# Optimization experiments

Hardware: AMD Instinct MI355X
Metric: run time of the kernel (lower is better)

Reference implementation:

```python
import jax, jax.numpy as jnp
import numpy as np

H = 512   # hidden_size
E = 256   # embedding_size
V = 32000 # vocab_size
L = 1024  # max_length (encoder seq len)
B = 64    # batch


def setup_inputs() -> dict:
    key = jax.random.key(0)
    ks = jax.random.split(key, 18)
    n = lambda i, shape, s=0.05: (jax.random.normal(ks[i], shape, dtype=jnp.float32) * s)
    return {
        "input": jax.random.randint(ks[0], (B, 1), 0, V),
        "last_output_context": n(1, (1, B, H), 1.0),
        "last_hidden": n(2, (1, B, H), 1.0),
        "last_cell_state": n(3, (1, B, H), 1.0),
        "encoder_outputs": n(4, (L, B, H), 1.0),
        "emb": n(5, (V, E)),
        "W_ih": n(6, (4 * H, E + H)),
        "W_hh": n(7, (4 * H, H)),
        "b_ih": n(8, (4 * H,)),
        "b_hh": n(9, (4 * H,)),
        "W_attn": n(10, (H, 2 * H)),
        "b_attn": n(11, (H,)),
        "beta": n(12, (H, 1), 1.0),
        "W_oc": n(13, (H, 2 * H)),
        "b_oc": n(14, (H,)),
        "W_out": n(15, (V, H)),
        "b_out": n(16, (V,)),
    }


def reference(input, last_output_context, last_hidden, last_cell_state,
              encoder_outputs, emb, W_ih, W_hh, b_ih, b_hh,
              W_attn, b_attn, beta, W_oc, b_oc, W_out, b_out):
    # embedding lookup: (B,1) -> (B,E)  (permute(1,0,2) then squeeze step dim)
    tok = emb[input[:, 0]]                                   # (B, E)
    x = jnp.concatenate([tok, last_output_context[0]], axis=1)  # (B, E+H)
    # single-step LSTM (PyTorch gate order i, f, g, o)
    gates = x @ W_ih.T + last_hidden[0] @ W_hh.T + b_ih + b_hh  # (B, 4H)
    i_g, f_g, g_g, o_g = jnp.split(gates, 4, axis=1)
    i_g = jax.nn.sigmoid(i_g)
    f_g = jax.nn.sigmoid(f_g)
    g_g = jnp.tanh(g_g)
    o_g = jax.nn.sigmoid(o_g)
    c = f_g * last_cell_state[0] + i_g * g_g                  # (B, H)
    h = o_g * jnp.tanh(c)                                     # (B, H) == rnn_output
    # additive attention, vectorized over the seq_len loop
    h_tiled = jnp.broadcast_to(h[None], (L, B, H))
    cat = jnp.concatenate([h_tiled, encoder_outputs], axis=-1)  # (L, B, 2H)
    energy = jnp.tanh(cat @ W_attn.T + b_attn) @ beta           # (L, B, 1)
    attn_w = jax.nn.softmax(energy[..., 0], axis=0)             # (L, B) softmax over seq
    # context = bmm(attn_weights, encoder_outputs)
    context = jnp.einsum('lb,lbh->bh', attn_w, encoder_outputs)  # (B, H)
    co = jnp.tanh(jnp.concatenate([h, context], axis=1) @ W_oc.T + b_oc)  # (B, H)
    output = jax.nn.log_softmax(co @ W_out.T + b_out, axis=1)    # (B, V)
    return output, co[None], h[None], c[None]
```

## Files before the change

### kernel.cpp

```cpp
#include <hip/hip_runtime.h>
#include <hip/hip_bf16.h>
#include <cstddef>

#define H   512
#define E   256
#define V   32000
#define L   1024
#define B   64
#define KX  768
#define M_TOT 65536

typedef __attribute__((ext_vector_type(8))) _Float16 half8v;
typedef __attribute__((ext_vector_type(4))) float f32x4;

__device__ __forceinline__ half8v cvt8(float4 x0, float4 x1) {
    union { half8v v; _Float16 u[8]; } hv;
    hv.u[0] = (_Float16)x0.x; hv.u[1] = (_Float16)x0.y;
    hv.u[2] = (_Float16)x0.z; hv.u[3] = (_Float16)x0.w;
    hv.u[4] = (_Float16)x1.x; hv.u[5] = (_Float16)x1.y;
    hv.u[6] = (_Float16)x1.z; hv.u[7] = (_Float16)x1.w;
    return hv.v;
}

__global__ __launch_bounds__(256) void k_conv_w(const float* __restrict__ W_attn,
                                                unsigned short* __restrict__ Wf) {
    int e0 = blockIdx.x * 2048 + threadIdx.x * 8;
    int j = e0 >> 9, k = e0 & 511;
    const float* src = &W_attn[(size_t)j * (2 * H) + H + k];
    float4 x0 = *reinterpret_cast<const float4*>(src);
    float4 x1 = *reinterpret_cast<const float4*>(src + 4);
    half8v hv = cvt8(x0, x1);
    *reinterpret_cast<half8v*>(&Wf[e0]) = hv;
}

__global__ __launch_bounds__(256) void k_build(const int* __restrict__ inp,
                                               const float* __restrict__ loc,
                                               const float* __restrict__ hprev,
                                               const float* __restrict__ emb,
                                               float* __restrict__ xprevT) {
    int gid = blockIdx.x * 256 + threadIdx.x;
    int k = gid >> 6, b = gid & 63;
    float v;
    if (k < 256)      v = emb[(size_t)inp[b] * E + k];
    else if (k < 768) v = loc[b * H + (k - 256)];
    else              v = hprev[b * H + (k - 768)];
    xprevT[gid] = v;
}

__global__ __launch_bounds__(256) void k_lstm(const float* __restrict__ W_ih,
                                              const float* __restrict__ W_hh,
                                              const float* __restrict__ b_ih,
                                              const float* __restrict__ b_hh,
                                              const float* __restrict__ xprevT,
                                              const float* __restrict__ cprev,
                                              float* __restrict__ h_out,
                                              float* __restrict__ c_out,
                                              float* __restrict__ hnewT) {
    int u = blockIdx.x;
    int w = threadIdx.x >> 6;
    int b = threadIdx.x & 63;
    int j = w * 512 + u;
    float a0 = 0.f, a1 = 0.f, a2 = 0.f, a3 = 0.f;
    const float* Wr = &W_ih[(size_t)j * KX];
    for (int k = 0; k < KX; k += 4) {
        float4 wv = *reinterpret_cast<const float4*>(&Wr[k]);
        a0 += wv.x * xprevT[(k + 0) * 64 + b];
        a1 += wv.y * xprevT[(k + 1) * 64 + b];
        a2 += wv.z * xprevT[(k + 2) * 64 + b];
        a3 += wv.w * xprevT[(k + 3) * 64 + b];
    }
    const float* Wr2 = &W_hh[(size_t)j * H];
    const float* hT = &xprevT[KX * 64];
    for (int k = 0; k < H; k += 4) {
        float4 wv = *reinterpret_cast<const float4*>(&Wr2[k]);
        a0 += wv.x * hT[(k + 0) * 64 + b];
        a1 += wv.y * hT[(k + 1) * 64 + b];
        a2 += wv.z * hT[(k + 2) * 64 + b];
        a3 += wv.w * hT[(k + 3) * 64 + b];
    }
    float acc = b_ih[j] + b_hh[j] + ((a0 + a1) + (a2 + a3));
    __shared__ float gs[4][64];
    gs[w][b] = acc;
    __syncthreads();
    if (threadIdx.x < 64) {
        float ig = 1.f / (1.f + __expf(-gs[0][b]));
        float fg = 1.f / (1.f + __expf(-gs[1][b]));
        float gg = tanhf(gs[2][b]);
        float og = 1.f / (1.f + __expf(-gs[3][b]));
        float c = fg * cprev[b * H + u] + ig * gg;
        float h = og * tanhf(c);
        c_out[b * H + u] = c;
        h_out[b * H + u] = h;
        hnewT[u * 64 + b] = h;
    }
}

__global__ __launch_bounds__(256) void k_hw(const float* __restrict__ W_attn,
                                            const float* __restrict__ b_attn,
                                            const float* __restrict__ hT,
                                            float* __restrict__ hW_jb) {
    int j = blockIdx.x * 4 + (threadIdx.x >> 6);
    int b = threadIdx.x & 63;
    float a0 = 0.f, a1 = 0.f, a2 = 0.f, a3 = 0.f;
    const float* Wr = &W_attn[(size_t)j * (2 * H)];
    for (int k = 0; k < H; k += 4) {
        float4 wv = *reinterpret_cast<const float4*>(&Wr[k]);
        a0 += wv.x * hT[(k + 0) * 64 + b];
        a1 += wv.y * hT[(k + 1) * 64 + b];
        a2 += wv.z * hT[(k + 2) * 64 + b];
        a3 += wv.w * hT[(k + 3) * 64 + b];
    }
    hW_jb[j * 64 + b] = b_attn[j] + ((a0 + a1) + (a2 + a3));
}

#define BKE 32
#define PITCH 40

__global__ __launch_bounds__(256, 4) void k_energy_v7(
        const float* __restrict__ enc,
        const unsigned short* __restrict__ Wf,
        const float* __restrict__ hW,
        const float* __restrict__ beta,
        float* __restrict__ partial_e) {
    __shared__ unsigned short Ah[128 * PITCH];
    __shared__ unsigned short Bh[128 * PITCH];
    __shared__ float red[2][128];

    const int tid  = threadIdx.x;
    const int lane = tid & 63;
    const int wave = tid >> 6;
    const int wm = wave >> 1;
    const int wn = wave & 1;
    const int bid = blockIdx.x;
    const int xcd = bid & 7;
    const int loc = bid >> 3;
    const int mt  = xcd * 64 + (loc >> 2);
    const int jt  = loc & 3;
    const int m0 = mt * 128;
    const int j0 = jt * 128;

    const int srow = tid >> 2;
    const int skc  = tid & 3;

    float4 ra0[2], ra1[2];
    half8v rb[2];
    #pragma unroll
    for (int p = 0; p < 2; ++p) {
        int row = p * 64 + srow;
        const float* asrc = &enc[(size_t)(m0 + row) * H + skc * 8];
        ra0[p] = *reinterpret_cast<const float4*>(asrc);
        ra1[p] = *reinterpret_cast<const float4*>(asrc + 4);
        rb[p] = *reinterpret_cast<const half8v*>(&Wf[(size_t)(j0 + row) * H + skc * 8]);
    }

    f32x4 acc[4][4];
    #pragma unroll
    for (int i = 0; i < 4; ++i)
        #pragma unroll
        for (int j = 0; j < 4; ++j) acc[i][j] = (f32x4){0.f, 0.f, 0.f, 0.f};

    for (int k0 = 0; k0 < H; k0 += BKE) {
        __syncthreads();
        #pragma unroll
        for (int p = 0; p < 2; ++p) {
            half8v hv = cvt8(ra0[p], ra1[p]);
            int off = (p * 64 + srow) * PITCH + skc * 8;
            *reinterpret_cast<half8v*>(&Ah[off]) = hv;
            *reinterpret_cast<half8v*>(&Bh[off]) = rb[p];
        }
        __syncthreads();
        if (k0 + BKE < H) {
            int kn = k0 + BKE;
            #pragma unroll
            for (int p = 0; p < 2; ++p) {
                int row = p * 64 + srow;
                const float* asrc = &enc[(size_t)(m0 + row) * H + kn + skc * 8];
                ra0[p] = *reinterpret_cast<const float4*>(asrc);
                ra1[p] = *reinterpret_cast<const float4*>(asrc + 4);
                rb[p] = *reinterpret_cast<const half8v*>(&Wf[(size_t)(j0 + row) * H + kn + skc * 8]);
            }
        }
        const int fr = lane & 15;
        const int kb = (lane >> 4) * 8;
        half8v a_h[4], b_h[4];
        #pragma unroll
        for (int mf = 0; mf < 4; ++mf) {
            int off = (wm * 64 + mf * 16 + fr) * PITCH + kb;
            a_h[mf] = *reinterpret_cast<const half8v*>(&Ah[off]);
        }
        #pragma unroll
        for (int nf = 0; nf < 4; ++nf) {
            int off = (wn * 64 + nf * 16 + fr) * PITCH + kb;
            b_h[nf] = *reinterpret_cast<const half8v*>(&Bh[off]);
        }
        #pragma unroll
        for (int mf = 0; mf < 4; ++mf)
            #pragma unroll
            for (int nf = 0; nf < 4; ++nf)
                acc[mf][nf] = __builtin_amdgcn_mfma_f32_16x16x32_f16(
                    a_h[mf], b_h[nf], acc[mf][nf], 0, 0, 0);
    }
    float psum[4][4];
    #pragma unroll
    for (int i = 0; i < 4; ++i)
        #pragma unroll
        for (int r = 0; r < 4; ++r) psum[i][r] = 0.f;
    #pragma unroll
    for (int nf = 0; nf < 4; ++nf) {
        int jj = j0 + wn * 64 + nf * 16 + (lane & 15);
        float bet = beta[jj];
        #pragma unroll
        for (int mf = 0; mf < 4; ++mf) {
            int b_base = (wm * 64 + mf * 16 + (lane >> 4) * 4) & 63;
            float4 hw4 = *reinterpret_cast<const float4*>(&hW[jj * 64 + b_base]);
            float hwv[4] = {hw4.x, hw4.y, hw4.z, hw4.w};
            #pragma unroll
            for (int r = 0; r < 4; ++r) {
                float e = acc[mf][nf][r] + hwv[r];
                float ex = __expf(2.f * e);
                psum[mf][r] += bet * (1.f - 2.f / (ex + 1.f));
            }
        }
    }
    #pragma unroll
    for (int mf = 0; mf < 4; ++mf)
        #pragma unroll
        for (int r = 0; r < 4; ++r) {
            float v = psum[mf][r];
            v += __shfl_xor(v, 1);
            v += __shfl_xor(v, 2);
            v += __shfl_xor(v, 4);
            v += __shfl_xor(v, 8);
            psum[mf][r] = v;
        }
    __syncthreads();
    if ((lane & 15) == 0) {
        #pragma unroll
        for (int mf = 0; mf < 4; ++mf)
            #pragma unroll
            for (int r = 0; r < 4; ++r)
                red[wn][wm * 64 + mf * 16 + (lane >> 4) * 4 + r] = psum[mf][r];
    }
    __syncthreads();
    if (tid < 128)
        partial_e[(size_t)jt * M_TOT + m0 + tid] = red[0][tid] + red[1][tid];
}

__global__ __launch_bounds__(256) void k_softmax_l(const float* __restrict__ partial_e,
                                                   float* __restrict__ attn_w) {
    int b = blockIdx.x;
    int tid = threadIdx.x;
    float el[4];
    float m = -1e30f;
    #pragma unroll
    for (int i = 0; i < 4; ++i) {
        int l = i * 256 + tid;
        float e = 0.f;
        #pragma unroll
        for (int nb = 0; nb < 4; ++nb)
            e += partial_e[(size_t)nb * M_TOT + l * 64 + b];
        el[i] = e;
        m = fmaxf(m, e);
    }
    #pragma unroll
    for (int s = 1; s < 64; s <<= 1) m = fmaxf(m, __shfl_xor(m, s));
    __shared__ float redm[4];
    if ((tid & 63) == 0) redm[tid >> 6] = m;
    __syncthreads();
    m = fmaxf(fmaxf(redm[0], redm[1]), fmaxf(redm[2], redm[3]));
    float s = 0.f;
    #pragma unroll
    for (int i = 0; i < 4; ++i) { el[i] = __expf(el[i] - m); s += el[i]; }
    #pragma unroll
    for (int sh = 1; sh < 64; sh <<= 1) s += __shfl_xor(s, sh);
    __shared__ float reds[4];
    if ((tid & 63) == 0) reds[tid >> 6] = s;
    __syncthreads();
    s = reds[0] + reds[1] + reds[2] + reds[3];
    float inv = 1.f / s;
    #pragma unroll
    for (int i = 0; i < 4; ++i)
        attn_w[(i * 256 + tid) * 64 + b] = el[i] * inv;
}

__global__ __launch_bounds__(128) void k_ctx_part(const float* __restrict__ attn_w,
                                                  const float* __restrict__ enc,
                                                  float* __restrict__ ctx_part) {
    int chunk = blockIdx.x, b = blockIdx.y;
    int h = threadIdx.x * 4;
    float4 acc = {0.f, 0.f, 0.f, 0.f};
    for (int i = 0; i < 32; ++i) {
        int l = chunk * 32 + i;
        float w = attn_w[l * 64 + b];
        float4 e4 = *reinterpret_cast<const float4*>(
            &enc[((size_t)l * 64 + b) * H + h]);
        acc.x += w * e4.x;
        acc.y += w * e4.y;
        acc.z += w * e4.z;
        acc.w += w * e4.w;
    }
    *reinterpret_cast<float4*>(&ctx_part[((size_t)(chunk * 64 + b)) * H + h]) = acc;
}

__global__ __launch_bounds__(256) void k_ctx_reduce(const float* __restrict__ ctx_part,
                                                    float* __restrict__ ctxT) {
    int gid = blockIdx.x * 256 + threadIdx.x;
    int b = gid >> 9, h = gid & 511;
    float s = 0.f;
    for (int c = 0; c < 32; ++c)
        s += ctx_part[((size_t)(c * 64 + b)) * H + h];
    ctxT[h * 64 + b] = s;
}

__global__ __launch_bounds__(256) void k_co(const float* __restrict__ W_oc,
                                            const float* __restrict__ b_oc,
                                            const float* __restrict__ hT,
                                            const float* __restrict__ ctxT,
                                            float* __restrict__ co_out) {
    int j = blockIdx.x * 4 + (threadIdx.x >> 6);
    int b = threadIdx.x & 63;
    float a0 = 0.f, a1 = 0.f, a2 = 0.f, a3 = 0.f;
    const float* Wr = &W_oc[(size_t)j * (2 * H)];
    for (int k = 0; k < H; k += 4) {
        float4 wv = *reinterpret_cast<const float4*>(&Wr[k]);
        a0 += wv.x * hT[(k + 0) * 64 + b];
        a1 += wv.y * hT[(k + 1) * 64 + b];
        a2 += wv.z * hT[(k + 2) * 64 + b];
        a3 += wv.w * hT[(k + 3) * 64 + b];
    }
    const float* Wr2 = Wr + H;
    for (int k = 0; k < H; k += 4) {
        float4 wv = *reinterpret_cast<const float4*>(&Wr2[k]);
        a0 += wv.x * ctxT[(k + 0) * 64 + b];
        a1 += wv.y * ctxT[(k + 1) * 64 + b];
        a2 += wv.z * ctxT[(k + 2) * 64 + b];
        a3 += wv.w * ctxT[(k + 3) * 64 + b];
    }
    co_out[b * H + j] = tanhf(b_oc[j] + ((a0 + a1) + (a2 + a3)));
}

__global__ __launch_bounds__(256) void k_logits_v3(const float* __restrict__ co,
                                                   const float* __restrict__ W_out,
                                                   const float* __restrict__ b_out,
                                                   float* __restrict__ logits) {
    const int tid  = threadIdx.x;
    const int lane = tid & 63;
    const int w    = tid >> 6;
    const int fr   = lane & 15;
    const int kb   = (lane >> 4) * 8;
    const int j    = blockIdx.x * 64 + w * 16 + fr;

    f32x4 acc[4];
    #pragma unroll
    for (int mf = 0; mf < 4; ++mf) acc[mf] = (f32x4){0.f, 0.f, 0.f, 0.f};

    const float* Arow = &co[(size_t)fr * H + kb];
    const float* Brow = &W_out[(size_t)j * H + kb];

    for (int k0 = 0; k0 < H; k0 += 32) {
        float4 b0 = *reinterpret_cast<const float4*>(Brow + k0);
        float4 b1 = *reinterpret_cast<const float4*>(Brow + k0 + 4);
        half8v bh = cvt8(b0, b1);
        #pragma unroll
        for (int mf = 0; mf < 4; ++mf) {
            const float* ap = Arow + (size_t)mf * 16 * H + k0;
            float4 a0 = *reinterpret_cast<const float4*>(ap);
            float4 a1 = *reinterpret_cast<const float4*>(ap + 4);
            half8v ah = cvt8(a0, a1);
            acc[mf] = __builtin_amdgcn_mfma_f32_16x16x32_f16(ah, bh, acc[mf], 0, 0, 0);
        }
    }
    float bo = b_out[j];
    #pragma unroll
    for (int mf = 0; mf < 4; ++mf) {
        int mbase = mf * 16 + (lane >> 4) * 4;
        #pragma unroll
        for (int r = 0; r < 4; ++r)
            logits[(size_t)(mbase + r) * V + j] = acc[mf][r] + bo;
    }
}

__global__ __launch_bounds__(256) void k_lsm_part(const float* __restrict__ logits,
                                                  float* __restrict__ pmax,
                                                  float* __restrict__ psum) {
    int chunk = blockIdx.x, b = blockIdx.y;
    int tid = threadIdx.x;
    const float* row = &logits[(size_t)b * V + chunk * 4000];
    float v[16];
    float m = -1e30f;
    #pragma unroll
    for (int t = 0; t < 16; ++t) {
        int i = t * 256 + tid;
        v[t] = (i < 4000) ? row[i] : -1e30f;
        m = fmaxf(m, v[t]);
    }
    #pragma unroll
    for (int s = 1; s < 64; s <<= 1) m = fmaxf(m, __shfl_xor(m, s));
    __shared__ float redm[4];
    if ((tid & 63) == 0) redm[tid >> 6] = m;
    __syncthreads();
    m = fmaxf(fmaxf(redm[0], redm[1]), fmaxf(redm[2], redm[3]));
    float s = 0.f;
    #pragma unroll
    for (int t = 0; t < 16; ++t) s += __expf(v[t] - m);
    #pragma unroll
    for (int sh = 1; sh < 64; sh <<= 1) s += __shfl_xor(s, sh);
    __shared__ float reds[4];
    if ((tid & 63) == 0) reds[tid >> 6] = s;
    __syncthreads();
    if (tid == 0) {
        pmax[chunk * 64 + b] = m;
        psum[chunk * 64 + b] = reds[0] + reds[1] + reds[2] + reds[3];
    }
}

__global__ __launch_bounds__(64) void k_lsm_final(const float* __restrict__ pmax,
                                                  const float* __restrict__ psum,
                                                  float* __restrict__ lse) {
    int b = threadIdx.x;
    float m = -1e30f;
    #pragma unroll
    for (int c = 0; c < 8; ++c) m = fmaxf(m, pmax[c * 64 + b]);
    float s = 0.f;
    #pragma unroll
    for (int c = 0; c < 8; ++c) s += psum[c * 64 + b] * __expf(pmax[c * 64 + b] - m);
    lse[b] = m + __logf(s);
}

__global__ __launch_bounds__(256) void k_lsm_write(const float* __restrict__ logits,
                                                   const float* __restrict__ lse,
                                                   float* __restrict__ out) {
    size_t i4 = ((size_t)blockIdx.x * 256 + threadIdx.x) * 4;
    int b = (int)(i4 / V);
    float l = lse[b];
    float4 x = *reinterpret_cast<const float4*>(&logits[i4]);
    x.x -= l; x.y -= l; x.z -= l; x.w -= l;
    *reinterpret_cast<float4*>(&out[i4]) = x;
}

extern "C" void kernel_launch(void* const* d_in, const int* in_sizes, int n_in,
                              void* d_out, int out_size, void* d_ws, size_t ws_size,
                              hipStream_t stream) {
    const int*   inp    = (const int*)  d_in[0];
    const float* loc    = (const float*)d_in[1];
    const float* hprev  = (const float*)d_in[2];
    const float* cprev  = (const float*)d_in[3];
    const float* enc    = (const float*)d_in[4];
    const float* emb    = (const float*)d_in[5];
    const float* W_ih   = (const float*)d_in[6];
    const float* W_hh   = (const float*)d_in[7];
    const float* b_ih   = (const float*)d_in[8];
    const float* b_hh   = (const float*)d_in[9];
    const float* W_attn = (const float*)d_in[10];
    const float* b_attn = (const float*)d_in[11];
    const float* beta   = (const float*)d_in[12];
    const float* W_oc   = (const float*)d_in[13];
    const float* b_oc   = (const float*)d_in[14];
    const float* W_out  = (const float*)d_in[15];
    const float* b_out  = (const float*)d_in[16];

    float* out = (float*)d_out;
    float* out_co = out + (size_t)B * V;
    float* out_h  = out_co + B * H;
    float* out_c  = out_h  + B * H;

    float* ws = (float*)d_ws;
    float* xprevT = ws;
    float* hnewT  = xprevT + 1280 * 64;
    float* hW     = hnewT  + H * 64;
    float* pe     = hW     + H * 64;
    float* attnw  = pe     + 4 * M_TOT;
    float* ctxp   = attnw  + M_TOT;
    float* ctxT   = ctxp   + 32 * 64 * H;
    float* logits = ctxT   + H * 64;
    float* pmax   = logits + (size_t)B * V;
    float* psum   = pmax   + 512;
    float* lse    = psum   + 512;
    unsigned short* Wf = (unsigned short*)(lse + 64);

    k_conv_w<<<128, 256, 0, stream>>>(W_attn, Wf);
    k_build <<<320, 256, 0, stream>>>(inp, loc, hprev, emb, xprevT);
    k_lstm  <<<512, 256, 0, stream>>>(W_ih, W_hh, b_ih, b_hh, xprevT, cprev,
                                      out_h, out_c, hnewT);
    k_hw    <<<128, 256, 0, stream>>>(W_attn, b_attn, hnewT, hW);
    k_energy_v7<<<2048, 256, 0, stream>>>(enc, Wf, hW, beta, pe);
    k_softmax_l<<<64, 256, 0, stream>>>(pe, attnw);
    k_ctx_part <<<dim3(32, 64), 128, 0, stream>>>(attnw, enc, ctxp);
    k_ctx_reduce<<<128, 256, 0, stream>>>(ctxp, ctxT);
    k_co    <<<128, 256, 0, stream>>>(W_oc, b_oc, hnewT, ctxT, out_co);
    k_logits_v3<<<500, 256, 0, stream>>>(out_co, W_out, b_out, logits);
    k_lsm_part<<<dim3(8, 64), 256, 0, stream>>>(logits, pmax, psum);
    k_lsm_final<<<1, 64, 0, stream>>>(pmax, psum, lse);
    k_lsm_write<<<2000, 256, 0, stream>>>(logits, lse, out);
}
```

Baseline: 254.8 us.

## Double-buffer LDS tiles in energy GEMM with two register prefetch stages

Reworks the attention-energy MFMA kernel to use two LDS buffers and two sets of prefetch registers, so global loads for step k+2 and LDS writes for step k+1 overlap with MFMA work on step k. This removes one of the two barriers per K-step and fully unrolls the K loop. In exchange it doubles LDS use and raises register pressure, and the launch bound drops from 4 to 3 blocks per SIMD, which may lower occupancy.

```diff
diff --git a/kernel.cpp b/kernel.cpp
--- a/kernel.cpp
+++ b/kernel.cpp
@@ -115,15 +115,16 @@
 
 #define BKE 32
 #define PITCH 40
-
-__global__ __launch_bounds__(256, 4) void k_energy_v7(
+#define LDSOFF (128 * PITCH)
+
+__global__ __launch_bounds__(256, 3) void k_energy_v8(
         const float* __restrict__ enc,
         const unsigned short* __restrict__ Wf,
         const float* __restrict__ hW,
         const float* __restrict__ beta,
         float* __restrict__ partial_e) {
-    __shared__ unsigned short Ah[128 * PITCH];
-    __shared__ unsigned short Bh[128 * PITCH];
+    __shared__ unsigned short Ah[2 * LDSOFF];
+    __shared__ unsigned short Bh[2 * LDSOFF];
     __shared__ float red[2][128];
 
     const int tid  = threadIdx.x;
@@ -141,16 +142,34 @@
 
     const int srow = tid >> 2;
     const int skc  = tid & 3;
-
-    float4 ra0[2], ra1[2];
-    half8v rb[2];
-    #pragma unroll
-    for (int p = 0; p < 2; ++p) {
-        int row = p * 64 + srow;
-        const float* asrc = &enc[(size_t)(m0 + row) * H + skc * 8];
-        ra0[p] = *reinterpret_cast<const float4*>(asrc);
-        ra1[p] = *reinterpret_cast<const float4*>(asrc + 4);
-        rb[p] = *reinterpret_cast<const half8v*>(&Wf[(size_t)(j0 + row) * H + skc * 8]);
+    const int soff = srow * PITCH + skc * 8;
+    const int soff2 = (64 + srow) * PITCH + skc * 8;
+
+    const float*          Abase = &enc[(size_t)m0 * H + skc * 8];
+    const unsigned short* Bbase = &Wf[(size_t)j0 * H + skc * 8];
+    const size_t arow = (size_t)srow * H, arow2 = (size_t)(64 + srow) * H;
+
+    float4 r0a0, r0a1, r0c0, r0c1; half8v r0b0, r0b1;
+    float4 r1a0, r1a1, r1c0, r1c1; half8v r1b0, r1b1;
+
+#define LOADSET(Ra0, Ra1, Rc0, Rc1, Rb0, Rb1, kk)                               \
+    {                                                                           \
+        const float* a1p = Abase + arow + (kk);                                 \
+        const float* a2p = Abase + arow2 + (kk);                                \
+        Ra0 = *reinterpret_cast<const float4*>(a1p);                            \
+        Ra1 = *reinterpret_cast<const float4*>(a1p + 4);                        \
+        Rc0 = *reinterpret_cast<const float4*>(a2p);                            \
+        Rc1 = *reinterpret_cast<const float4*>(a2p + 4);                        \
+        Rb0 = *reinterpret_cast<const half8v*>(&Bbase[arow + (kk)]);            \
+        Rb1 = *reinterpret_cast<const half8v*>(&Bbase[arow2 + (kk)]);           \
+    }
+
+#define WRITESET(Ra0, Ra1, Rc0, Rc1, Rb0, Rb1, sbuf)                            \
+    {                                                                           \
+        *reinterpret_cast<half8v*>(&Ah[(sbuf) + soff])  = cvt8(Ra0, Ra1);       \
+        *reinterpret_cast<half8v*>(&Ah[(sbuf) + soff2]) = cvt8(Rc0, Rc1);       \
+        *reinterpret_cast<half8v*>(&Bh[(sbuf) + soff])  = Rb0;                  \
+        *reinterpret_cast<half8v*>(&Bh[(sbuf) + soff2]) = Rb1;                  \
     }
 
     f32x4 acc[4][4];
@@ -159,47 +178,50 @@
         #pragma unroll
         for (int j = 0; j < 4; ++j) acc[i][j] = (f32x4){0.f, 0.f, 0.f, 0.f};
 
-    for (int k0 = 0; k0 < H; k0 += BKE) {
+    const int fr = lane & 15;
+    const int kb = (lane >> 4) * 8;
+    const int aoffm = (wm * 64 + fr) * PITCH + kb;
+    const int boffn = (wn * 64 + fr) * PITCH + kb;
+
+#define CONSUME(sbuf)                                                           \
+    {                                                                           \
+        half8v a_h[4], b_h[4];                                                  \
+        _Pragma("unroll")                                                       \
+        for (int mf = 0; mf < 4; ++mf)                                          \
+            a_h[mf] = *reinterpret_cast<const half8v*>(                         \
+                &Ah[(sbuf) + aoffm + mf * (16 * PITCH)]);                       \
+        _Pragma("unroll")                                                       \
+        for (int nf = 0; nf < 4; ++nf)                                          \
+            b_h[nf] = *reinterpret_cast<const half8v*>(                         \
+                &Bh[(sbuf) + boffn + nf * (16 * PITCH)]);                       \
+        _Pragma("unroll")                                                       \
+        for (int mf = 0; mf < 4; ++mf)                                          \
+            _Pragma("unroll")                                                   \
+            for (int nf = 0; nf < 4; ++nf)                                      \
+                acc[mf][nf] = __builtin_amdgcn_mfma_f32_16x16x32_f16(           \
+                    a_h[mf], b_h[nf], acc[mf][nf], 0, 0, 0);                    \
+    }
+
+    LOADSET(r0a0, r0a1, r0c0, r0c1, r0b0, r0b1, 0)
+    LOADSET(r1a0, r1a1, r1c0, r1c1, r1b0, r1b1, BKE)
+    WRITESET(r0a0, r0a1, r0c0, r0c1, r0b0, r0b1, 0)
+    __syncthreads();
+
+    #pragma unroll
+    for (int jj = 0; jj < 8; ++jj) {
+        const int k0 = jj * 64;
+        if (k0 + 64 < H) LOADSET(r0a0, r0a1, r0c0, r0c1, r0b0, r0b1, k0 + 64)
+        WRITESET(r1a0, r1a1, r1c0, r1c1, r1b0, r1b1, LDSOFF)
+        CONSUME(0)
         __syncthreads();
-        #pragma unroll
-        for (int p = 0; p < 2; ++p) {
-            half8v hv = cvt8(ra0[p], ra1[p]);
-            int off = (p * 64 + srow) * PITCH + skc * 8;
-            *reinterpret_cast<half8v*>(&Ah[off]) = hv;
-            *reinterpret_cast<half8v*>(&Bh[off]) = rb[p];
+        if (k0 + 96 < H) LOADSET(r1a0, r1a1, r1c0, r1c1, r1b0, r1b1, k0 + 96)
+        if (k0 + 64 < H) {
+            WRITESET(r0a0, r0a1, r0c0, r0c1, r0b0, r0b1, 0)
         }
+        CONSUME(LDSOFF)
         __syncthreads();
-        if (k0 + BKE < H) {
-            int kn = k0 + BKE;
-            #pragma unroll
-            for (int p = 0; p < 2; ++p) {
-                int row = p * 64 + srow;
-                const float* asrc = &enc[(size_t)(m0 + row) * H + kn + skc * 8];
-                ra0[p] = *reinterpret_cast<const float4*>(asrc);
-                ra1[p] = *reinterpret_cast<const float4*>(asrc + 4);
-                rb[p] = *reinterpret_cast<const half8v*>(&Wf[(size_t)(j0 + row) * H + kn + skc * 8]);
-            }
-        }
-        const int fr = lane & 15;
-        const int kb = (lane >> 4) * 8;
-        half8v a_h[4], b_h[4];
-        #pragma unroll
-        for (int mf = 0; mf < 4; ++mf) {
-            int off = (wm * 64 + mf * 16 + fr) * PITCH + kb;
-            a_h[mf] = *reinterpret_cast<const half8v*>(&Ah[off]);
-        }
-        #pragma unroll
-        for (int nf = 0; nf < 4; ++nf) {
-            int off = (wn * 64 + nf * 16 + fr) * PITCH + kb;
-            b_h[nf] = *reinterpret_cast<const half8v*>(&Bh[off]);
-        }
-        #pragma unroll
-        for (int mf = 0; mf < 4; ++mf)
-            #pragma unroll
-            for (int nf = 0; nf < 4; ++nf)
-                acc[mf][nf] = __builtin_amdgcn_mfma_f32_16x16x32_f16(
-                    a_h[mf], b_h[nf], acc[mf][nf], 0, 0, 0);
-    }
+    }
+
     float psum[4][4];
     #pragma unroll
     for (int i = 0; i < 4; ++i)
@@ -207,12 +229,12 @@
         for (int r = 0; r < 4; ++r) psum[i][r] = 0.f;
     #pragma unroll
     for (int nf = 0; nf < 4; ++nf) {
-        int jj = j0 + wn * 64 + nf * 16 + (lane & 15);
-        float bet = beta[jj];
+        int jjx = j0 + wn * 64 + nf * 16 + (lane & 15);
+        float bet = beta[jjx];
         #pragma unroll
         for (int mf = 0; mf < 4; ++mf) {
             int b_base = (wm * 64 + mf * 16 + (lane >> 4) * 4) & 63;
-            float4 hw4 = *reinterpret_cast<const float4*>(&hW[jj * 64 + b_base]);
+            float4 hw4 = *reinterpret_cast<const float4*>(&hW[jjx * 64 + b_base]);
             float hwv[4] = {hw4.x, hw4.y, hw4.z, hw4.w};
             #pragma unroll
             for (int r = 0; r < 4; ++r) {
@@ -483,7 +505,7 @@
     k_lstm  <<<512, 256, 0, stream>>>(W_ih, W_hh, b_ih, b_hh, xprevT, cprev,
                                       out_h, out_c, hnewT);
     k_hw    <<<128, 256, 0, stream>>>(W_attn, b_attn, hnewT, hW);
-    k_energy_v7<<<2048, 256, 0, stream>>>(enc, Wf, hW, beta, pe);
+    k_energy_v8<<<2048, 256, 0, stream>>>(enc, Wf, hW, beta, pe);
     k_softmax_l<<<64, 256, 0, stream>>>(pe, attnw);
     k_ctx_part <<<dim3(32, 64), 128, 0, stream>>>(attnw, enc, ctxp);
     k_ctx_reduce<<<128, 256, 0, stream>>>(ctxp, ctxT);
```

New measurement: 262.6 us. +3.0%, slower.

## Pre-convert encoder outputs to tiled fp16 and load tiles directly into LDS

Applied to the files above, without the earlier changes.

Adds a pass that converts encoder_outputs and the attention weight half into fp16 arranged in per-tile contiguous blocks. The energy GEMM then streams these tiles straight into shared memory with global_load_lds instead of loading fp32 into registers, converting and storing. This removes the in-loop conversion and register staging, but adds a full extra read/write pass over the encoder tensor and drops the register-level prefetch overlap and LDS padding.

```diff
diff --git a/kernel.cpp b/kernel.cpp
--- a/kernel.cpp
+++ b/kernel.cpp
@@ -22,15 +22,41 @@
     return hv.v;
 }
 
-__global__ __launch_bounds__(256) void k_conv_w(const float* __restrict__ W_attn,
-                                                unsigned short* __restrict__ Wf) {
-    int e0 = blockIdx.x * 2048 + threadIdx.x * 8;
-    int j = e0 >> 9, k = e0 & 511;
-    const float* src = &W_attn[(size_t)j * (2 * H) + H + k];
+__device__ __forceinline__ void glds16(const unsigned short* g, unsigned short* l) {
+    __builtin_amdgcn_global_load_lds(
+        (const __attribute__((address_space(1))) void*)g,
+        (__attribute__((address_space(3))) void*)l, 16, 0, 0);
+}
+
+__global__ __launch_bounds__(256) void k_conv_enc(const float* __restrict__ enc,
+                                                  unsigned short* __restrict__ encT) {
+    size_t u = (size_t)blockIdx.x * 256 + threadIdx.x;
+    int s = (int)(u & 3);
+    size_t rowg = u >> 2;
+    int row = (int)(rowg & 127);
+    size_t mtkt = rowg >> 7;
+    int kt = (int)(mtkt & 15);
+    size_t mt = mtkt >> 4;
+    const float* src = &enc[(mt * 128 + row) * 512 + kt * 32 + s * 8];
     float4 x0 = *reinterpret_cast<const float4*>(src);
     float4 x1 = *reinterpret_cast<const float4*>(src + 4);
-    half8v hv = cvt8(x0, x1);
-    *reinterpret_cast<half8v*>(&Wf[e0]) = hv;
+    *reinterpret_cast<half8v*>(&encT[u * 8]) = cvt8(x0, x1);
+}
+
+__global__ __launch_bounds__(256) void k_conv_w2(const float* __restrict__ W_attn,
+                                                 unsigned short* __restrict__ WfT) {
+    int u = blockIdx.x * 256 + threadIdx.x;
+    int s = u & 3;
+    int rowg = u >> 2;
+    int row = rowg & 127;
+    int jtkt = rowg >> 7;
+    int kt = jtkt & 15;
+    int jt = jtkt >> 4;
+    int j = jt * 128 + row;
+    const float* src = &W_attn[(size_t)j * (2 * H) + H + kt * 32 + s * 8];
+    float4 x0 = *reinterpret_cast<const float4*>(src);
+    float4 x1 = *reinterpret_cast<const float4*>(src + 4);
+    *reinterpret_cast<half8v*>(&WfT[u * 8]) = cvt8(x0, x1);
 }
 
 __global__ __launch_bounds__(256) void k_build(const int* __restrict__ inp,
@@ -113,24 +139,21 @@
     hW_jb[j * 64 + b] = b_attn[j] + ((a0 + a1) + (a2 + a3));
 }
 
-#define BKE 32
-#define PITCH 40
-
-__global__ __launch_bounds__(256, 4) void k_energy_v7(
-        const float* __restrict__ enc,
-        const unsigned short* __restrict__ Wf,
+__global__ __launch_bounds__(256, 4) void k_energy_v9(
+        const unsigned short* __restrict__ encT,
+        const unsigned short* __restrict__ WfT,
         const float* __restrict__ hW,
         const float* __restrict__ beta,
         float* __restrict__ partial_e) {
-    __shared__ unsigned short Ah[128 * PITCH];
-    __shared__ unsigned short Bh[128 * PITCH];
+    __shared__ unsigned short Ah[128 * 32];
+    __shared__ unsigned short Bh[128 * 32];
     __shared__ float red[2][128];
 
     const int tid  = threadIdx.x;
     const int lane = tid & 63;
-    const int wave = tid >> 6;
-    const int wm = wave >> 1;
-    const int wn = wave & 1;
+    const int w    = tid >> 6;
+    const int wm = w >> 1;
+    const int wn = w & 1;
     const int bid = blockIdx.x;
     const int xcd = bid & 7;
     const int loc = bid >> 3;
@@ -139,19 +162,10 @@
     const int m0 = mt * 128;
     const int j0 = jt * 128;
 
-    const int srow = tid >> 2;
-    const int skc  = tid & 3;
-
-    float4 ra0[2], ra1[2];
-    half8v rb[2];
-    #pragma unroll
-    for (int p = 0; p < 2; ++p) {
-        int row = p * 64 + srow;
-        const float* asrc = &enc[(size_t)(m0 + row) * H + skc * 8];
-        ra0[p] = *reinterpret_cast<const float4*>(asrc);
-        ra1[p] = *reinterpret_cast<const float4*>(asrc + 4);
-        rb[p] = *reinterpret_cast<const half8v*>(&Wf[(size_t)(j0 + row) * H + skc * 8]);
-    }
+    const unsigned short* Ag = encT + (size_t)mt * (16 * 4096) + w * 1024 + lane * 8;
+    const unsigned short* Bg = WfT  + (size_t)jt * (16 * 4096) + w * 1024 + lane * 8;
+    unsigned short* Al = &Ah[w * 1024];
+    unsigned short* Bl = &Bh[w * 1024];
 
     f32x4 acc[4][4];
     #pragma unroll
@@ -159,47 +173,34 @@
         #pragma unroll
         for (int j = 0; j < 4; ++j) acc[i][j] = (f32x4){0.f, 0.f, 0.f, 0.f};
 
-    for (int k0 = 0; k0 < H; k0 += BKE) {
+    const int fr = lane & 15;
+    const int s8 = (lane >> 4) * 8;
+
+    for (int kt = 0; kt < 16; ++kt) {
+        const int g0 = kt * 4096;
+        glds16(Ag + g0,       Al);
+        glds16(Ag + g0 + 512, Al + 512);
+        glds16(Bg + g0,       Bl);
+        glds16(Bg + g0 + 512, Bl + 512);
         __syncthreads();
-        #pragma unroll
-        for (int p = 0; p < 2; ++p) {
-            half8v hv = cvt8(ra0[p], ra1[p]);
-            int off = (p * 64 + srow) * PITCH + skc * 8;
-            *reinterpret_cast<half8v*>(&Ah[off]) = hv;
-            *reinterpret_cast<half8v*>(&Bh[off]) = rb[p];
-        }
-        __syncthreads();
-        if (k0 + BKE < H) {
-            int kn = k0 + BKE;
-            #pragma unroll
-            for (int p = 0; p < 2; ++p) {
-                int row = p * 64 + srow;
-                const float* asrc = &enc[(size_t)(m0 + row) * H + kn + skc * 8];
-                ra0[p] = *reinterpret_cast<const float4*>(asrc);
-                ra1[p] = *reinterpret_cast<const float4*>(asrc + 4);
-                rb[p] = *reinterpret_cast<const half8v*>(&Wf[(size_t)(j0 + row) * H + kn + skc * 8]);
-            }
-        }
-        const int fr = lane & 15;
-        const int kb = (lane >> 4) * 8;
         half8v a_h[4], b_h[4];
         #pragma unroll
-        for (int mf = 0; mf < 4; ++mf) {
-            int off = (wm * 64 + mf * 16 + fr) * PITCH + kb;
-            a_h[mf] = *reinterpret_cast<const half8v*>(&Ah[off]);
-        }
-        #pragma unroll
-        for (int nf = 0; nf < 4; ++nf) {
-            int off = (wn * 64 + nf * 16 + fr) * PITCH + kb;
-            b_h[nf] = *reinterpret_cast<const half8v*>(&Bh[off]);
-        }
+        for (int mf = 0; mf < 4; ++mf)
+            a_h[mf] = *reinterpret_cast<const half8v*>(
+                &Ah[(wm * 64 + mf * 16 + fr) * 32 + s8]);
+        #pragma unroll
+        for (int nf = 0; nf < 4; ++nf)
+            b_h[nf] = *reinterpret_cast<const half8v*>(
+                &Bh[(wn * 64 + nf * 16 + fr) * 32 + s8]);
         #pragma unroll
         for (int mf = 0; mf < 4; ++mf)
             #pragma unroll
             for (int nf = 0; nf < 4; ++nf)
                 acc[mf][nf] = __builtin_amdgcn_mfma_f32_16x16x32_f16(
                     a_h[mf], b_h[nf], acc[mf][nf], 0, 0, 0);
-    }
+        __syncthreads();
+    }
+
     float psum[4][4];
     #pragma unroll
     for (int i = 0; i < 4; ++i)
@@ -476,14 +477,16 @@
     float* pmax   = logits + (size_t)B * V;
     float* psum   = pmax   + 512;
     float* lse    = psum   + 512;
-    unsigned short* Wf = (unsigned short*)(lse + 64);
-
-    k_conv_w<<<128, 256, 0, stream>>>(W_attn, Wf);
+    unsigned short* WfT  = (unsigned short*)(lse + 64);
+    unsigned short* encT = WfT + (size_t)H * H;
+
+    k_conv_w2<<<128, 256, 0, stream>>>(W_attn, WfT);
     k_build <<<320, 256, 0, stream>>>(inp, loc, hprev, emb, xprevT);
     k_lstm  <<<512, 256, 0, stream>>>(W_ih, W_hh, b_ih, b_hh, xprevT, cprev,
                                       out_h, out_c, hnewT);
     k_hw    <<<128, 256, 0, stream>>>(W_attn, b_attn, hnewT, hW);
-    k_energy_v7<<<2048, 256, 0, stream>>>(enc, Wf, hW, beta, pe);
+    k_conv_enc<<<16384, 256, 0, stream>>>(enc, encT);
+    k_energy_v9<<<2048, 256, 0, stream>>>(encT, WfT, hW, beta, pe);
     k_softmax_l<<<64, 256, 0, stream>>>(pe, attnw);
     k_ctx_part <<<dim3(32, 64), 128, 0, stream>>>(attnw, enc, ctxp);
     k_ctx_reduce<<<128, 256, 0, stream>>>(ctxp, ctxT);
```

After: 292.2 us. +14.7%, slower.

## Use direct global-to-LDS loads with MFMA-fragment layout in energy GEMM

Applied to the files above, without the earlier changes.

The energy GEMM kernel now loads encoder fp32 tiles and pre-swizzled fp16 W_attn tiles straight into shared memory with global_load_lds, instead of staging them through registers. The fp16 conversion of the encoder tile moves to the point where fragments are read from LDS. The W_attn conversion kernel writes weights in MFMA fragment order so B fragments are contiguous per lane. The K step grows from 32 to 64 and occupancy drops from 4 to 3 blocks per CU, trading the register prefetch pipeline for larger LDS tiles with no double buffering.

```diff
diff --git a/kernel.cpp b/kernel.cpp
--- a/kernel.cpp
+++ b/kernel.cpp
@@ -22,15 +22,25 @@
     return hv.v;
 }
 
-__global__ __launch_bounds__(256) void k_conv_w(const float* __restrict__ W_attn,
-                                                unsigned short* __restrict__ Wf) {
-    int e0 = blockIdx.x * 2048 + threadIdx.x * 8;
-    int j = e0 >> 9, k = e0 & 511;
-    const float* src = &W_attn[(size_t)j * (2 * H) + H + k];
+__device__ __forceinline__ void glds16(const void* g, void* l) {
+    __builtin_amdgcn_global_load_lds(
+        (const __attribute__((address_space(1))) void*)g,
+        (__attribute__((address_space(3))) void*)l, 16, 0, 0);
+}
+
+__global__ __launch_bounds__(256) void k_conv_w3(const float* __restrict__ W_attn,
+                                                 unsigned short* __restrict__ WfB) {
+    int u = blockIdx.x * 256 + threadIdx.x;
+    int lane = u & 63;
+    int rest = u >> 6;
+    int kh = rest & 1, nf = (rest >> 1) & 3, wn = (rest >> 3) & 1;
+    int kt2 = (rest >> 4) & 7, jt = rest >> 7;
+    int j = jt * 128 + wn * 64 + nf * 16 + (lane & 15);
+    int col = kt2 * 64 + kh * 32 + (lane >> 4) * 8;
+    const float* src = &W_attn[(size_t)j * (2 * H) + H + col];
     float4 x0 = *reinterpret_cast<const float4*>(src);
     float4 x1 = *reinterpret_cast<const float4*>(src + 4);
-    half8v hv = cvt8(x0, x1);
-    *reinterpret_cast<half8v*>(&Wf[e0]) = hv;
+    *reinterpret_cast<half8v*>(&WfB[(size_t)u * 8]) = cvt8(x0, x1);
 }
 
 __global__ __launch_bounds__(256) void k_build(const int* __restrict__ inp,
@@ -113,24 +123,21 @@
     hW_jb[j * 64 + b] = b_attn[j] + ((a0 + a1) + (a2 + a3));
 }
 
-#define BKE 32
-#define PITCH 40
-
-__global__ __launch_bounds__(256, 4) void k_energy_v7(
+__global__ __launch_bounds__(256, 3) void k_energy_v11(
         const float* __restrict__ enc,
-        const unsigned short* __restrict__ Wf,
+        const unsigned short* __restrict__ WfB,
         const float* __restrict__ hW,
         const float* __restrict__ beta,
         float* __restrict__ partial_e) {
-    __shared__ unsigned short Ah[128 * PITCH];
-    __shared__ unsigned short Bh[128 * PITCH];
+    __shared__ float Af[8192];
+    __shared__ unsigned short Bh[8192];
     __shared__ float red[2][128];
 
     const int tid  = threadIdx.x;
     const int lane = tid & 63;
-    const int wave = tid >> 6;
-    const int wm = wave >> 1;
-    const int wn = wave & 1;
+    const int w    = tid >> 6;
+    const int wm = w >> 1;
+    const int wn = w & 1;
     const int bid = blockIdx.x;
     const int xcd = bid & 7;
     const int loc = bid >> 3;
@@ -139,19 +146,22 @@
     const int m0 = mt * 128;
     const int j0 = jt * 128;
 
-    const int srow = tid >> 2;
-    const int skc  = tid & 3;
-
-    float4 ra0[2], ra1[2];
-    half8v rb[2];
-    #pragma unroll
-    for (int p = 0; p < 2; ++p) {
-        int row = p * 64 + srow;
-        const float* asrc = &enc[(size_t)(m0 + row) * H + skc * 8];
-        ra0[p] = *reinterpret_cast<const float4*>(asrc);
-        ra1[p] = *reinterpret_cast<const float4*>(asrc + 4);
-        rb[p] = *reinterpret_cast<const half8v*>(&Wf[(size_t)(j0 + row) * H + skc * 8]);
-    }
+    const int fr = lane & 15;
+    const int g  = lane >> 4;
+
+    const float* asrc[8];
+    #pragma unroll
+    for (int i = 0; i < 8; ++i) {
+        int idx2 = w * 8 + i;
+        int q  = idx2 >> 2;
+        int kh = (idx2 >> 1) & 1;
+        int c  = idx2 & 1;
+        int row = q * 16 + fr;
+        int col = kh * 32 + g * 8 + c * 4;
+        asrc[i] = enc + (size_t)(m0 + row) * H + col;
+    }
+    const unsigned short* bsrc = WfB + (size_t)jt * 65536
+                               + ((size_t)(w * 4) * 64 + lane) * 8;
 
     f32x4 acc[4][4];
     #pragma unroll
@@ -159,47 +169,41 @@
         #pragma unroll
         for (int j = 0; j < 4; ++j) acc[i][j] = (f32x4){0.f, 0.f, 0.f, 0.f};
 
-    for (int k0 = 0; k0 < H; k0 += BKE) {
+    for (int kt2 = 0; kt2 < 8; ++kt2) {
+        #pragma unroll
+        for (int i = 0; i < 8; ++i)
+            glds16(asrc[i] + kt2 * 64, &Af[(w * 8 + i) * 256 + lane * 4]);
+        #pragma unroll
+        for (int i = 0; i < 4; ++i)
+            glds16(bsrc + (size_t)kt2 * 8192 + i * 512,
+                   &Bh[((w * 4 + i) * 64 + lane) * 8]);
         __syncthreads();
         #pragma unroll
-        for (int p = 0; p < 2; ++p) {
-            half8v hv = cvt8(ra0[p], ra1[p]);
-            int off = (p * 64 + srow) * PITCH + skc * 8;
-            *reinterpret_cast<half8v*>(&Ah[off]) = hv;
-            *reinterpret_cast<half8v*>(&Bh[off]) = rb[p];
+        for (int kh = 0; kh < 2; ++kh) {
+            half8v a_h[4], b_h[4];
+            #pragma unroll
+            for (int mf = 0; mf < 4; ++mf) {
+                int q = wm * 4 + mf;
+                int cb = ((q * 2 + kh) * 2) * 256 + lane * 4;
+                float4 f0 = *reinterpret_cast<const float4*>(&Af[cb]);
+                float4 f1 = *reinterpret_cast<const float4*>(&Af[cb + 256]);
+                a_h[mf] = cvt8(f0, f1);
+            }
+            #pragma unroll
+            for (int nf = 0; nf < 4; ++nf) {
+                int cb = (((wn * 4 + nf) * 2 + kh) * 64 + lane) * 8;
+                b_h[nf] = *reinterpret_cast<const half8v*>(&Bh[cb]);
+            }
+            #pragma unroll
+            for (int mf = 0; mf < 4; ++mf)
+                #pragma unroll
+                for (int nf = 0; nf < 4; ++nf)
+                    acc[mf][nf] = __builtin_amdgcn_mfma_f32_16x16x32_f16(
+                        a_h[mf], b_h[nf], acc[mf][nf], 0, 0, 0);
         }
         __syncthreads();
-        if (k0 + BKE < H) {
-            int kn = k0 + BKE;
-            #pragma unroll
-            for (int p = 0; p < 2; ++p) {
-                int row = p * 64 + srow;
-                const float* asrc = &enc[(size_t)(m0 + row) * H + kn + skc * 8];
-                ra0[p] = *reinterpret_cast<const float4*>(asrc);
-                ra1[p] = *reinterpret_cast<const float4*>(asrc + 4);
-                rb[p] = *reinterpret_cast<const half8v*>(&Wf[(size_t)(j0 + row) * H + kn + skc * 8]);
-            }
-        }
-        const int fr = lane & 15;
-        const int kb = (lane >> 4) * 8;
-        half8v a_h[4], b_h[4];
-        #pragma unroll
-        for (int mf = 0; mf < 4; ++mf) {
-            int off = (wm * 64 + mf * 16 + fr) * PITCH + kb;
-            a_h[mf] = *reinterpret_cast<const half8v*>(&Ah[off]);
-        }
-        #pragma unroll
-        for (int nf = 0; nf < 4; ++nf) {
-            int off = (wn * 64 + nf * 16 + fr) * PITCH + kb;
-            b_h[nf] = *reinterpret_cast<const half8v*>(&Bh[off]);
-        }
-        #pragma unroll
-        for (int mf = 0; mf < 4; ++mf)
-            #pragma unroll
-            for (int nf = 0; nf < 4; ++nf)
-                acc[mf][nf] = __builtin_amdgcn_mfma_f32_16x16x32_f16(
-                    a_h[mf], b_h[nf], acc[mf][nf], 0, 0, 0);
-    }
+    }
+
     float psum[4][4];
     #pragma unroll
     for (int i = 0; i < 4; ++i)
@@ -476,14 +480,14 @@
     float* pmax   = logits + (size_t)B * V;
     float* psum   = pmax   + 512;
     float* lse    = psum   + 512;
-    unsigned short* Wf = (unsigned short*)(lse + 64);
-
-    k_conv_w<<<128, 256, 0, stream>>>(W_attn, Wf);
+    unsigned short* WfB = (unsigned short*)(lse + 64);
+
+    k_conv_w3<<<128, 256, 0, stream>>>(W_attn, WfB);
     k_build <<<320, 256, 0, stream>>>(inp, loc, hprev, emb, xprevT);
     k_lstm  <<<512, 256, 0, stream>>>(W_ih, W_hh, b_ih, b_hh, xprevT, cprev,
                                       out_h, out_c, hnewT);
     k_hw    <<<128, 256, 0, stream>>>(W_attn, b_attn, hnewT, hW);
-    k_energy_v7<<<2048, 256, 0, stream>>>(enc, Wf, hW, beta, pe);
+    k_energy_v11<<<2048, 256, 0, stream>>>(enc, WfB, hW, beta, pe);
     k_softmax_l<<<64, 256, 0, stream>>>(pe, attnw);
     k_ctx_part <<<dim3(32, 64), 128, 0, stream>>>(attnw, enc, ctxp);
     k_ctx_reduce<<<128, 256, 0, stream>>>(ctxp, ctxT);
```

After: 284.4 us. +11.6%, slower.
